# Kernel tuning notes

Measured on AMD Instinct MI355X. Metric: run time of the kernel, lower is better.

The kernel has to match this reference:

```python
import jax, jax.numpy as jnp
import numpy as np

B, T, V, E, H, L = 32, 512, 50000, 256, 512, 50
FORGET_BIAS = 1.0


def setup_inputs() -> dict:
    key = jax.random.key(0)
    ks = jax.random.split(key, 8)
    q = jax.random.randint(ks[0], (B, T), 0, V, dtype=jnp.int32)
    a = jax.random.randint(ks[1], (B, T), 0, L, dtype=jnp.int32)
    lengths = jax.random.randint(ks[2], (B,), 1, T + 1, dtype=jnp.int32)
    word_embed = jax.random.normal(ks[3], (V, E), jnp.float32) * 0.1
    lstm_W = jax.random.normal(ks[4], (E + H, 4 * H), jnp.float32) * (1.0 / np.sqrt(E + H))
    lstm_b = jnp.zeros((4 * H,), jnp.float32)
    proj_W = jax.random.normal(ks[5], (H, L), jnp.float32) * (1.0 / np.sqrt(H))
    proj_b = jnp.zeros((L,), jnp.float32)
    return {"q": q, "a": a, "lengths": lengths, "word_embed": word_embed,
            "lstm_W": lstm_W, "lstm_b": lstm_b, "proj_W": proj_W, "proj_b": proj_b}


def _lstm(emb, lengths, W, b):
    # emb: [B, T, E] -> outputs [B, T, H]; BasicLSTMCell gate order i, j, f, o
    xs = emb.transpose(1, 0, 2)                                   # [T, B, E]
    mt = (jnp.arange(emb.shape[1])[:, None] < lengths[None, :]).astype(emb.dtype)[:, :, None]  # [T, B, 1]
    h_dim = W.shape[1] // 4
    init = (jnp.zeros((emb.shape[0], h_dim), emb.dtype),
            jnp.zeros((emb.shape[0], h_dim), emb.dtype))

    def step(carry, inp):
        c, h = carry
        x, m = inp
        z = jnp.concatenate([x, h], axis=-1) @ W + b              # [B, 4H]
        i, j, f, o = jnp.split(z, 4, axis=-1)
        c_new = c * jax.nn.sigmoid(f + FORGET_BIAS) + jax.nn.sigmoid(i) * jnp.tanh(j)
        h_new = jnp.tanh(c_new) * jax.nn.sigmoid(o)
        # dynamic_rnn: past sequence_length, output is zero and state is copied through
        c2 = m * c_new + (1.0 - m) * c
        h2 = m * h_new + (1.0 - m) * h
        return (c2, h2), m * h_new

    _, ys = jax.lax.scan(step, init, (xs, mt))
    return ys.transpose(1, 0, 2)                                  # [B, T, H]


def reference(q, a, lengths, word_embed, lstm_W, lstm_b, proj_W, proj_b):
    emb = word_embed[q]                                           # [B, T, E]
    outputs = _lstm(emb, lengths, lstm_W, lstm_b)                 # [B, T, H]
    logits = jax.nn.relu(outputs.reshape(-1, outputs.shape[-1]) @ proj_W + proj_b)  # [B*T, L]
    labels = a.reshape(-1)
    mask = (jnp.arange(q.shape[1])[None, :] < lengths[:, None]).astype(jnp.float32).reshape(-1)
    logp = jax.nn.log_softmax(logits, axis=-1)
    xent = -jnp.take_along_axis(logp, labels[:, None], axis=-1)[:, 0] * mask  # [B*T]
    losses = xent.reshape(q.shape)                                # [B, T]
    losses_per_seq = losses.sum(axis=1) / lengths.astype(jnp.float32)
    loss = losses_per_seq.sum() / q.shape[0]
    return loss
```

## Files before the change

### kernel.cpp

```cpp
#include <hip/hip_runtime.h>
#include <hip/hip_bf16.h>

#define B_ 32
#define T_ 512
#define E_ 256
#define H_ 512
#define L_ 50
#define V_ 50000
#define NBLK 32
#define NGRID 32

typedef __attribute__((ext_vector_type(8))) short short8;
typedef __attribute__((ext_vector_type(4))) float v4f;
typedef __attribute__((ext_vector_type(4))) int i4;
typedef unsigned long long u64;

__device__ __forceinline__ unsigned short f2bf(float f){
    union { float f; unsigned u; } v; v.f = f;
    unsigned u = v.u;
    u += 0x7fffu + ((u >> 16) & 1u);
    return (unsigned short)(u >> 16);
}
__device__ __forceinline__ float fastsig(float x){
    return __builtin_amdgcn_rcpf(1.0f + __expf(-x));
}
__device__ __forceinline__ float fasttanh(float x){
    return 1.0f - 2.0f * __builtin_amdgcn_rcpf(__expf(2.0f * x) + 1.0f);
}

__device__ __forceinline__ float qredmax(float v){
    v = fmaxf(v, __shfl_xor(v, 1, 64));
    v = fmaxf(v, __shfl_xor(v, 2, 64));
    v = fmaxf(v, __shfl_xor(v, 4, 64));
    v = fmaxf(v, __shfl_xor(v, 8, 64));
    return v;
}
__device__ __forceinline__ float qredsum(float v){
    v += __shfl_xor(v, 1, 64);
    v += __shfl_xor(v, 2, 64);
    v += __shfl_xor(v, 4, 64);
    v += __shfl_xor(v, 8, 64);
    return v;
}

__device__ __forceinline__ i4 load16_dev(const void* p){
    i4 r;
    asm volatile("global_load_dwordx4 %0, %1, off sc0 sc1" : "=v"(r) : "v"(p) : "memory");
    return r;
}
__device__ __forceinline__ void store8_dev(void* p, u64 v){
    asm volatile("global_store_dwordx2 %0, %1, off sc0 sc1" : : "v"(p), "v"(v) : "memory");
}
__device__ __forceinline__ void store4_dev(void* p, unsigned v){
    asm volatile("global_store_dword %0, %1, off sc0 sc1" : : "v"(p), "v"(v) : "memory");
}
__device__ __forceinline__ unsigned load4_dev_wait(const void* p){
    unsigned r;
    asm volatile("global_load_dword %0, %1, off sc0 sc1\n\ts_waitcnt vmcnt(0)"
                 : "=v"(r) : "v"(p) : "memory");
    return r;
}
__device__ __forceinline__ void wait_vm0(){
    asm volatile("s_waitcnt vmcnt(0)" ::: "memory");
}

__global__ void init_kernel(const float* __restrict__ projW,
                            const float* __restrict__ we,
                            float* __restrict__ out,
                            unsigned int* __restrict__ setup,
                            unsigned int* __restrict__ flags,
                            unsigned short* __restrict__ h0,
                            unsigned short* __restrict__ Wt,
                            unsigned short* __restrict__ we_bf)
{
    const int i = blockIdx.x * 256 + threadIdx.x;
    if (i < 1024) setup[i] = 0u;
    if (i < NBLK) flags[i] = 0u;
    if (i == 0) out[0] = 0.f;
    if (i < B_ * H_) h0[i] = 0;
    if (i < 64 * H_){
        const int c = i >> 9;
        const int k = i & 511;
        const float v = (c < L_) ? projW[k * L_ + c] : 0.f;
        Wt[i] = f2bf(v);
    }
    if (i < (V_ * E_) / 8){
        const v4f* src = (const v4f*)(we + (size_t)i * 8);
        const v4f a = src[0], b = src[1];
        short8 o;
#pragma unroll
        for (int j = 0; j < 4; ++j){ o[j] = (short)f2bf(a[j]); o[4 + j] = (short)f2bf(b[j]); }
        *(short8*)(we_bf + (size_t)i * 8) = o;
    }
}

__global__ void __launch_bounds__(256, 1) lstm_kernel(
    const int* __restrict__ q, const int* __restrict__ lengths,
    const unsigned short* __restrict__ we_bf, const float* __restrict__ lstmW,
    const float* __restrict__ lstmB,
    unsigned short* __restrict__ h_all, unsigned int* __restrict__ flags)
{
    const int tid  = threadIdx.x;
    const int blk  = blockIdx.x;

    const int wv   = tid >> 6;
    const int lane = tid & 63;
    const int nt = wv & 1, mpair = wv >> 1;
    const int l15 = lane & 15, quad = lane >> 4;

    const int hcA0 = blk * 16 + (mpair * 2 + 0) * 4 + (l15 >> 2);
    const int hcA1 = blk * 16 + (mpair * 2 + 1) * 4 + (l15 >> 2);
    const int gA   = l15 & 3;
    const int colA0 = gA * H_ + hcA0;
    const int colA1 = gA * H_ + hcA1;

    short8 AW0[8], AW1[8], AH0[16], AH1[16];
#pragma unroll
    for (int kc = 0; kc < 8; ++kc){
        short8 f0, f1;
#pragma unroll
        for (int j = 0; j < 8; ++j){
            const int r = kc * 32 + quad * 8 + j;
            f0[j] = (short)f2bf(lstmW[(size_t)r * 2048 + colA0]);
            f1[j] = (short)f2bf(lstmW[(size_t)r * 2048 + colA1]);
        }
        AW0[kc] = f0; AW1[kc] = f1;
    }
#pragma unroll
    for (int kc = 0; kc < 16; ++kc){
        short8 f0, f1;
#pragma unroll
        for (int j = 0; j < 8; ++j){
            const int r = E_ + kc * 32 + quad * 8 + j;
            f0[j] = (short)f2bf(lstmW[(size_t)r * 2048 + colA0]);
            f1[j] = (short)f2bf(lstmW[(size_t)r * 2048 + colA1]);
        }
        AH0[kc] = f0; AH1[kc] = f1;
    }

    const int bE   = nt * 16 + l15;
    const int hcE0 = blk * 16 + (mpair * 2 + 0) * 4 + quad;
    const int hcE1 = blk * 16 + (mpair * 2 + 1) * 4 + quad;
    float bias0[4], bias1[4];
#pragma unroll
    for (int g = 0; g < 4; ++g){ bias0[g] = lstmB[g * H_ + hcE0]; bias1[g] = lstmB[g * H_ + hcE1]; }
    const int lenb = lengths[bE];

    float c0 = 0.f, c1 = 0.f, hp0 = 0.f, hp1 = 0.f;

    v4f accX0 = { bias0[0], bias0[1], bias0[2], bias0[3] };
    v4f accX1 = { bias1[0], bias1[1], bias1[2], bias1[3] };
    {
        const int qv = q[bE * T_];
        const short8* wp = (const short8*)(we_bf + (size_t)qv * E_);
#pragma unroll
        for (int kc = 0; kc < 8; ++kc){
            const short8 eb = wp[kc * 4 + quad];
            accX0 = __builtin_amdgcn_mfma_f32_16x16x32_bf16(AW0[kc], eb, accX0, 0, 0, 0);
            accX1 = __builtin_amdgcn_mfma_f32_16x16x32_bf16(AW1[kc], eb, accX1, 0, 0, 0);
        }
    }

    int qnext = q[bE * T_ + 1];

    for (int t = 0; t < T_; ++t){
        if (t > 0){
            int guard = 0;
            for (;;){
                unsigned f = 0xFFFFFFFFu;
                if (lane < NBLK) f = load4_dev_wait(flags + lane);
                if (__ballot(f >= (unsigned)t) == 0xFFFFFFFFFFFFFFFFull) break;
                __builtin_amdgcn_s_sleep(1);
                if (++guard > (1 << 16)) break;
            }
        }

        const unsigned short* hrow = h_all + (size_t)t * (B_ * H_) + (size_t)bE * H_;
        i4 hbuf[16];
#pragma unroll
        for (int kc = 0; kc < 16; ++kc)
            hbuf[kc] = load16_dev(hrow + kc * 32 + quad * 8);
        wait_vm0();

        short8 xe[8];
        {
            const short8* wp = (const short8*)(we_bf + (size_t)qnext * E_);
#pragma unroll
            for (int kc = 0; kc < 8; ++kc) xe[kc] = wp[kc * 4 + quad];
        }
        const int qnext2 = q[bE * T_ + ((t + 2 < T_) ? (t + 2) : (T_ - 1))];

        v4f a0e = accX0, a1e = accX1;
        v4f a0o = { 0.f, 0.f, 0.f, 0.f }, a1o = { 0.f, 0.f, 0.f, 0.f };
#pragma unroll
        for (int kc = 0; kc < 16; kc += 2){
            union { i4 i; short8 s; } cv0, cv1; cv0.i = hbuf[kc]; cv1.i = hbuf[kc + 1];
            a0e = __builtin_amdgcn_mfma_f32_16x16x32_bf16(AH0[kc],     cv0.s, a0e, 0, 0, 0);
            a1e = __builtin_amdgcn_mfma_f32_16x16x32_bf16(AH1[kc],     cv0.s, a1e, 0, 0, 0);
            a0o = __builtin_amdgcn_mfma_f32_16x16x32_bf16(AH0[kc + 1], cv1.s, a0o, 0, 0, 0);
            a1o = __builtin_amdgcn_mfma_f32_16x16x32_bf16(AH1[kc + 1], cv1.s, a1o, 0, 0, 0);
        }
        const v4f acc0 = a0e + a0o;
        const v4f acc1 = a1e + a1o;

        const bool msk = (t < lenb);
        const float cn0 = c0 * fastsig(acc0[2] + 1.0f) + fastsig(acc0[0]) * fasttanh(acc0[1]);
        const float hn0 = fasttanh(cn0) * fastsig(acc0[3]);
        c0 = msk ? cn0 : c0;
        const float h20 = msk ? hn0 : hp0; hp0 = h20;
        const float cn1 = c1 * fastsig(acc1[2] + 1.0f) + fastsig(acc1[0]) * fasttanh(acc1[1]);
        const float hn1 = fasttanh(cn1) * fastsig(acc1[3]);
        c1 = msk ? cn1 : c1;
        const float h21 = msk ? hn1 : hp1; hp1 = h21;

        const unsigned hv0 = f2bf(h20), hv1 = f2bf(h21);
        const int a0 = __shfl((int)hv0, l15, 64),      a1 = __shfl((int)hv0, l15 + 16, 64);
        const int a2 = __shfl((int)hv0, l15 + 32, 64), a3 = __shfl((int)hv0, l15 + 48, 64);
        const int b0 = __shfl((int)hv1, l15, 64),      b1 = __shfl((int)hv1, l15 + 16, 64);
        const int b2 = __shfl((int)hv1, l15 + 32, 64), b3 = __shfl((int)hv1, l15 + 48, 64);
        unsigned short* dstBase = h_all + (size_t)(t + 1) * (B_ * H_) + (size_t)bE * H_
                                + blk * 16 + mpair * 8;
        if (quad == 0){
            const u64 pk = (u64)(unsigned short)a0 | ((u64)(unsigned short)a1 << 16)
                         | ((u64)(unsigned short)a2 << 32) | ((u64)(unsigned short)a3 << 48);
            store8_dev(dstBase, pk);
        } else if (quad == 1){
            const u64 pk = (u64)(unsigned short)b0 | ((u64)(unsigned short)b1 << 16)
                         | ((u64)(unsigned short)b2 << 32) | ((u64)(unsigned short)b3 << 48);
            store8_dev(dstBase + 4, pk);
        }
        wait_vm0();
        __syncthreads();
        if (tid == 0)
            store4_dev(&flags[blk], (unsigned)(t + 1));

        if (t + 1 < T_){
            accX0 = (v4f){ bias0[0], bias0[1], bias0[2], bias0[3] };
            accX1 = (v4f){ bias1[0], bias1[1], bias1[2], bias1[3] };
#pragma unroll
            for (int kc = 0; kc < 8; ++kc){
                accX0 = __builtin_amdgcn_mfma_f32_16x16x32_bf16(AW0[kc], xe[kc], accX0, 0, 0, 0);
                accX1 = __builtin_amdgcn_mfma_f32_16x16x32_bf16(AW1[kc], xe[kc], accX1, 0, 0, 0);
            }
        }
        qnext = qnext2;
    }
}

__global__ void __launch_bounds__(256) loss_kernel(
    const int* __restrict__ a, const int* __restrict__ lengths,
    const float* __restrict__ projB,
    const unsigned short* __restrict__ h_all,
    const unsigned short* __restrict__ Wt,
    float* __restrict__ out)
{
    const int tid = threadIdx.x;
    const int wv = tid >> 6, lane = tid & 63;
    const int l15 = lane & 15, quad = lane >> 4;
    const int wgid = blockIdx.x * 4 + wv;
    const int row0 = wgid * 16;

    const int rowA = row0 + l15;
    const int bA = rowA >> 9, tA = rowA & 511;
    const unsigned short* hrow = h_all + ((size_t)(tA + 1) * B_ + bA) * H_;

    v4f acc[4] = { {0,0,0,0}, {0,0,0,0}, {0,0,0,0}, {0,0,0,0} };
#pragma unroll
    for (int kc = 0; kc < 16; ++kc){
        const short8 af = *(const short8*)(hrow + kc * 32 + quad * 8);
#pragma unroll
        for (int ntl = 0; ntl < 4; ++ntl){
            const short8 bf = *(const short8*)(Wt + (size_t)(ntl * 16 + l15) * H_ + kc * 32 + quad * 8);
            acc[ntl] = __builtin_amdgcn_mfma_f32_16x16x32_bf16(af, bf, acc[ntl], 0, 0, 0);
        }
    }

    float pb[4]; bool cv[4];
#pragma unroll
    for (int ntl = 0; ntl < 4; ++ntl){
        const int c = ntl * 16 + l15;
        cv[ntl] = (c < L_);
        pb[ntl] = cv[ntl] ? projB[c] : 0.f;
    }

#pragma unroll
    for (int r = 0; r < 4; ++r){
        const int row = row0 + quad * 4 + r;
        const int b = row >> 9, t = row & 511;
        const int len = lengths[b];
        const bool valid = (t < len);

        float lv[4];
#pragma unroll
        for (int ntl = 0; ntl < 4; ++ntl)
            lv[ntl] = fmaxf(acc[ntl][r] + pb[ntl], 0.f);

        float mx = -1e30f;
#pragma unroll
        for (int ntl = 0; ntl < 4; ++ntl) if (cv[ntl]) mx = fmaxf(mx, lv[ntl]);
        mx = qredmax(mx);
        float se = 0.f;
#pragma unroll
        for (int ntl = 0; ntl < 4; ++ntl) if (cv[ntl]) se += expf(lv[ntl] - mx);
        se = qredsum(se);
        const int lbl = a[row];
        float cand = 0.f;
#pragma unroll
        for (int ntl = 0; ntl < 4; ++ntl) if (ntl * 16 + l15 == lbl) cand = lv[ntl];
        const float llbl = qredsum(cand);

        if (valid && l15 == 0){
            const float xent = logf(se) + mx - llbl;
            atomicAdd(out, xent / ((float)len * 32.0f));
        }
    }
}

extern "C" void kernel_launch(void* const* d_in, const int* in_sizes, int n_in,
                              void* d_out, int out_size, void* d_ws, size_t ws_size,
                              hipStream_t stream)
{
    const int*   q   = (const int*)d_in[0];
    const int*   a   = (const int*)d_in[1];
    const int*   len = (const int*)d_in[2];
    const float* we  = (const float*)d_in[3];
    const float* lW  = (const float*)d_in[4];
    const float* lB  = (const float*)d_in[5];
    const float* pW  = (const float*)d_in[6];
    const float* pB  = (const float*)d_in[7];
    float* out = (float*)d_out;

    unsigned char* ws = (unsigned char*)d_ws;
    unsigned int*   setup = (unsigned int*)ws;
    unsigned int*   flags = (unsigned int*)(ws + 4096);
    unsigned short* h_all = (unsigned short*)(ws + 8192);
    unsigned short* Wt    = (unsigned short*)(ws + 8192 + (size_t)(T_ + 1) * B_ * H_ * 2);
    unsigned short* we_bf = (unsigned short*)(ws + 8192 + (size_t)(T_ + 1) * B_ * H_ * 2 + 65536);

    init_kernel<<<dim3(6400), dim3(256), 0, stream>>>(pW, we, out, setup, flags, h_all, Wt, we_bf);

    {
        const int* q_ = q; const int* len_ = len; const unsigned short* we_ = we_bf;
        const float* lW_ = lW; const float* lB_ = lB;
        unsigned short* h_ = h_all; unsigned int* f_ = flags;
        void* args[] = { (void*)&q_, (void*)&len_, (void*)&we_, (void*)&lW_,
                         (void*)&lB_, (void*)&h_, (void*)&f_ };
        hipLaunchCooperativeKernel((void*)lstm_kernel, dim3(NGRID), dim3(256),
                                   args, 0, stream);
    }

    loss_kernel<<<dim3(256), dim3(256), 0, stream>>>(a, len, pB, h_all, Wt, out);
}
```

Before: 2.425 ms.

## Use per-wavefront flags and prefetch flag poll to drop block barrier

Replaces the per-block flag, written after a __syncthreads, with one flag per wavefront (128 flags), so each wave signals on its own and the block barrier goes away. After signalling, each wave issues non-blocking flag loads whose values are checked at the top of the next step, and it falls back to the spin loop only if some producer is not ready yet. This cuts barrier cost and hides the poll latency behind the input-projection MFMAs. In exchange each poll reads four times as many flags, and the early prefetch may read stale values that force an extra spin.

```diff
diff --git a/kernel.cpp b/kernel.cpp
--- a/kernel.cpp
+++ b/kernel.cpp
@@ -9,6 +9,7 @@
 #define V_ 50000
 #define NBLK 32
 #define NGRID 32
+#define NWFLAG 128
 
 typedef __attribute__((ext_vector_type(8))) short short8;
 typedef __attribute__((ext_vector_type(4))) float v4f;
@@ -54,10 +55,9 @@
 __device__ __forceinline__ void store4_dev(void* p, unsigned v){
     asm volatile("global_store_dword %0, %1, off sc0 sc1" : : "v"(p), "v"(v) : "memory");
 }
-__device__ __forceinline__ unsigned load4_dev_wait(const void* p){
+__device__ __forceinline__ unsigned load4_dev_nowait(const void* p){
     unsigned r;
-    asm volatile("global_load_dword %0, %1, off sc0 sc1\n\ts_waitcnt vmcnt(0)"
-                 : "=v"(r) : "v"(p) : "memory");
+    asm volatile("global_load_dword %0, %1, off sc0 sc1" : "=v"(r) : "v"(p) : "memory");
     return r;
 }
 __device__ __forceinline__ void wait_vm0(){
@@ -75,7 +75,7 @@
 {
     const int i = blockIdx.x * 256 + threadIdx.x;
     if (i < 1024) setup[i] = 0u;
-    if (i < NBLK) flags[i] = 0u;
+    if (i < NWFLAG) flags[i] = 0u;
     if (i == 0) out[0] = 0.f;
     if (i < B_ * H_) h0[i] = 0;
     if (i < 64 * H_){
@@ -162,16 +162,26 @@
     }
 
     int qnext = q[bE * T_ + 1];
+    unsigned pv0 = 0u, pv1 = 0u;
 
     for (int t = 0; t < T_; ++t){
         if (t > 0){
-            int guard = 0;
-            for (;;){
-                unsigned f = 0xFFFFFFFFu;
-                if (lane < NBLK) f = load4_dev_wait(flags + lane);
-                if (__ballot(f >= (unsigned)t) == 0xFFFFFFFFFFFFFFFFull) break;
-                __builtin_amdgcn_s_sleep(1);
-                if (++guard > (1 << 16)) break;
+            wait_vm0();
+            if (__ballot(pv0 >= (unsigned)t && pv1 >= (unsigned)t) != 0xFFFFFFFFFFFFFFFFull){
+                int guard = 0;
+                for (;;){
+                    unsigned f0, f1;
+                    asm volatile(
+                        "global_load_dword %0, %2, off sc0 sc1\n\t"
+                        "global_load_dword %1, %3, off sc0 sc1\n\t"
+                        "s_waitcnt vmcnt(0)"
+                        : "=v"(f0), "=v"(f1)
+                        : "v"(flags + lane), "v"(flags + lane + 64) : "memory");
+                    if (__ballot(f0 >= (unsigned)t && f1 >= (unsigned)t) == 0xFFFFFFFFFFFFFFFFull)
+                        break;
+                    __builtin_amdgcn_s_sleep(1);
+                    if (++guard > (1 << 16)) break;
+                }
             }
         }
 
@@ -230,9 +240,13 @@
             store8_dev(dstBase + 4, pk);
         }
         wait_vm0();
-        __syncthreads();
-        if (tid == 0)
-            store4_dev(&flags[blk], (unsigned)(t + 1));
+        if (lane == 0)
+            store4_dev(&flags[blk * 4 + wv], (unsigned)(t + 1));
+
+        if (t + 1 < T_){
+            pv0 = load4_dev_nowait(flags + lane);
+            pv1 = load4_dev_nowait(flags + lane + 64);
+        }
 
         if (t + 1 < T_){
             accX0 = (v4f){ bias0[0], bias0[1], bias0[2], bias0[3] };
```

After: 3.603 ms. 1.49x slower.

## Replace per-step flag barrier with sentinel-poisoned hidden-state polling

Applied to the files above, without the earlier changes.

The per-block completion flags and the __syncthreads plus flag store after each step are removed. Instead, init fills the whole h_all history with 0xFFFF sentinels, and each step polls its h row directly until no sentinel halfwords remain, so the data itself acts as the readiness signal. This cuts a store-wait, a block barrier and a separate flag round-trip from the serial critical path of each timestep. The risk is that a valid bf16 value of 0xFFFF (a NaN) would hang until the guard expires, and polling re-reads the full 1 KB row. The loss kernel also batches its h loads up front.

```diff
diff --git a/kernel.cpp b/kernel.cpp
--- a/kernel.cpp
+++ b/kernel.cpp
@@ -51,15 +51,6 @@
 __device__ __forceinline__ void store8_dev(void* p, u64 v){
     asm volatile("global_store_dwordx2 %0, %1, off sc0 sc1" : : "v"(p), "v"(v) : "memory");
 }
-__device__ __forceinline__ void store4_dev(void* p, unsigned v){
-    asm volatile("global_store_dword %0, %1, off sc0 sc1" : : "v"(p), "v"(v) : "memory");
-}
-__device__ __forceinline__ unsigned load4_dev_wait(const void* p){
-    unsigned r;
-    asm volatile("global_load_dword %0, %1, off sc0 sc1\n\ts_waitcnt vmcnt(0)"
-                 : "=v"(r) : "v"(p) : "memory");
-    return r;
-}
 __device__ __forceinline__ void wait_vm0(){
     asm volatile("s_waitcnt vmcnt(0)" ::: "memory");
 }
@@ -67,17 +58,18 @@
 __global__ void init_kernel(const float* __restrict__ projW,
                             const float* __restrict__ we,
                             float* __restrict__ out,
-                            unsigned int* __restrict__ setup,
-                            unsigned int* __restrict__ flags,
-                            unsigned short* __restrict__ h0,
+                            unsigned short* __restrict__ h_all,
                             unsigned short* __restrict__ Wt,
                             unsigned short* __restrict__ we_bf)
 {
     const int i = blockIdx.x * 256 + threadIdx.x;
-    if (i < 1024) setup[i] = 0u;
-    if (i < NBLK) flags[i] = 0u;
     if (i == 0) out[0] = 0.f;
-    if (i < B_ * H_) h0[i] = 0;
+    if (i < B_ * H_) h_all[i] = 0;
+    if (i < (T_ * B_ * H_) / 8){
+        const short8 can = { (short)0xFFFF,(short)0xFFFF,(short)0xFFFF,(short)0xFFFF,
+                             (short)0xFFFF,(short)0xFFFF,(short)0xFFFF,(short)0xFFFF };
+        *(short8*)(h_all + (size_t)B_ * H_ + (size_t)i * 8) = can;
+    }
     if (i < 64 * H_){
         const int c = i >> 9;
         const int k = i & 511;
@@ -98,7 +90,7 @@
     const int* __restrict__ q, const int* __restrict__ lengths,
     const unsigned short* __restrict__ we_bf, const float* __restrict__ lstmW,
     const float* __restrict__ lstmB,
-    unsigned short* __restrict__ h_all, unsigned int* __restrict__ flags)
+    unsigned short* __restrict__ h_all)
 {
     const int tid  = threadIdx.x;
     const int blk  = blockIdx.x;
@@ -164,23 +156,31 @@
     int qnext = q[bE * T_ + 1];
 
     for (int t = 0; t < T_; ++t){
-        if (t > 0){
+        const unsigned short* hrow = h_all + (size_t)t * (B_ * H_) + (size_t)bE * H_;
+        i4 hbuf[16];
+        {
             int guard = 0;
             for (;;){
-                unsigned f = 0xFFFFFFFFu;
-                if (lane < NBLK) f = load4_dev_wait(flags + lane);
-                if (__ballot(f >= (unsigned)t) == 0xFFFFFFFFFFFFFFFFull) break;
-                __builtin_amdgcn_s_sleep(1);
-                if (++guard > (1 << 16)) break;
+#pragma unroll
+                for (int kc = 0; kc < 16; ++kc)
+                    hbuf[kc] = load16_dev(hrow + kc * 32 + quad * 8);
+                wait_vm0();
+                unsigned m0 = 0u, m1 = 0u, m2 = 0u, m3 = 0u;
+#pragma unroll
+                for (int kc = 0; kc < 16; ++kc){
+                    asm("v_pk_max_u16 %0, %0, %1" : "+v"(m0) : "v"(hbuf[kc][0]));
+                    asm("v_pk_max_u16 %0, %0, %1" : "+v"(m1) : "v"(hbuf[kc][1]));
+                    asm("v_pk_max_u16 %0, %0, %1" : "+v"(m2) : "v"(hbuf[kc][2]));
+                    asm("v_pk_max_u16 %0, %0, %1" : "+v"(m3) : "v"(hbuf[kc][3]));
+                }
+                asm("v_pk_max_u16 %0, %0, %1" : "+v"(m0) : "v"(m1));
+                asm("v_pk_max_u16 %0, %0, %1" : "+v"(m2) : "v"(m3));
+                asm("v_pk_max_u16 %0, %0, %1" : "+v"(m0) : "v"(m2));
+                const bool valid = ((m0 & 0xFFFFu) != 0xFFFFu) && ((m0 >> 16) != 0xFFFFu);
+                if (__ballot(valid) == 0xFFFFFFFFFFFFFFFFull) break;
+                if (++guard > (1 << 14)) break;
             }
         }
-
-        const unsigned short* hrow = h_all + (size_t)t * (B_ * H_) + (size_t)bE * H_;
-        i4 hbuf[16];
-#pragma unroll
-        for (int kc = 0; kc < 16; ++kc)
-            hbuf[kc] = load16_dev(hrow + kc * 32 + quad * 8);
-        wait_vm0();
 
         short8 xe[8];
         {
@@ -229,10 +229,6 @@
                          | ((u64)(unsigned short)b2 << 32) | ((u64)(unsigned short)b3 << 48);
             store8_dev(dstBase + 4, pk);
         }
-        wait_vm0();
-        __syncthreads();
-        if (tid == 0)
-            store4_dev(&flags[blk], (unsigned)(t + 1));
 
         if (t + 1 < T_){
             accX0 = (v4f){ bias0[0], bias0[1], bias0[2], bias0[3] };
@@ -264,14 +260,20 @@
     const int bA = rowA >> 9, tA = rowA & 511;
     const unsigned short* hrow = h_all + ((size_t)(tA + 1) * B_ + bA) * H_;
 
+    i4 afb[16];
+#pragma unroll
+    for (int kc = 0; kc < 16; ++kc)
+        afb[kc] = load16_dev(hrow + kc * 32 + quad * 8);
+    wait_vm0();
+
     v4f acc[4] = { {0,0,0,0}, {0,0,0,0}, {0,0,0,0}, {0,0,0,0} };
 #pragma unroll
     for (int kc = 0; kc < 16; ++kc){
-        const short8 af = *(const short8*)(hrow + kc * 32 + quad * 8);
+        union { i4 i; short8 s; } u; u.i = afb[kc];
 #pragma unroll
         for (int ntl = 0; ntl < 4; ++ntl){
             const short8 bf = *(const short8*)(Wt + (size_t)(ntl * 16 + l15) * H_ + kc * 32 + quad * 8);
-            acc[ntl] = __builtin_amdgcn_mfma_f32_16x16x32_bf16(af, bf, acc[ntl], 0, 0, 0);
+            acc[ntl] = __builtin_amdgcn_mfma_f32_16x16x32_bf16(u.s, bf, acc[ntl], 0, 0, 0);
         }
     }
 
@@ -331,20 +333,18 @@
     float* out = (float*)d_out;
 
     unsigned char* ws = (unsigned char*)d_ws;
-    unsigned int*   setup = (unsigned int*)ws;
-    unsigned int*   flags = (unsigned int*)(ws + 4096);
     unsigned short* h_all = (unsigned short*)(ws + 8192);
     unsigned short* Wt    = (unsigned short*)(ws + 8192 + (size_t)(T_ + 1) * B_ * H_ * 2);
     unsigned short* we_bf = (unsigned short*)(ws + 8192 + (size_t)(T_ + 1) * B_ * H_ * 2 + 65536);
 
-    init_kernel<<<dim3(6400), dim3(256), 0, stream>>>(pW, we, out, setup, flags, h_all, Wt, we_bf);
+    init_kernel<<<dim3(6400), dim3(256), 0, stream>>>(pW, we, out, h_all, Wt, we_bf);
 
     {
         const int* q_ = q; const int* len_ = len; const unsigned short* we_ = we_bf;
         const float* lW_ = lW; const float* lB_ = lB;
-        unsigned short* h_ = h_all; unsigned int* f_ = flags;
+        unsigned short* h_ = h_all;
         void* args[] = { (void*)&q_, (void*)&len_, (void*)&we_, (void*)&lW_,
-                         (void*)&lB_, (void*)&h_, (void*)&f_ };
+                         (void*)&lB_, (void*)&h_ };
         hipLaunchCooperativeKernel((void*)lstm_kernel, dim3(NGRID), dim3(256),
                                    args, 0, stream);
     }
```

Result: slower. 3.314 ms (+36.6%).
